# Optimization experiments

Hardware: AMD Instinct MI355X
Metric: run time of the kernel (lower is better)

## Reference

```python
import jax, jax.numpy as jnp
import numpy as np

LEAK = 0.95
NUM_STEPS = 10
THR = 1.0  # all layers get threshold = 1.0 in __init__

@jax.custom_vjp
def spike(x):
    # Surrogate_BP_Function.forward: heaviside(x > 0)
    return (x > 0).astype(x.dtype)

def _spike_fwd(x):
    return spike(x), x

def _spike_bwd(x, g):
    # backward: grad * 0.3 * relu(1 - |x|)
    return (g * 0.3 * jnp.maximum(1.0 - jnp.abs(x), 0.0),)

spike.defvjp(_spike_fwd, _spike_bwd)

def conv3x3(x, w):
    # stride 1, padding 1, no bias, NCHW / OIHW
    return jax.lax.conv_general_dilated(
        x, w, window_strides=(1, 1), padding=[(1, 1), (1, 1)],
        dimension_numbers=('NCHW', 'OIHW', 'NCHW'))

def avgpool2(x):
    b, c, h, w = x.shape
    return x.reshape(b, c, h // 2, 2, w // 2, 2).mean(axis=(3, 5))

def setup_inputs() -> dict:
    key = jax.random.key(0)
    ks = jax.random.split(key, 11)
    def w(k, shape, scale):
        return jax.random.normal(k, shape, dtype=jnp.float32) * scale
    inp = jax.random.normal(ks[0], (128, 3, 32, 32), dtype=jnp.float32)
    return {
        'inp': inp,
        'w1': w(ks[1], (64, 3, 3, 3), 0.35),
        'w2': w(ks[2], (64, 64, 3, 3), 0.1),
        'w3': w(ks[3], (128, 64, 3, 3), 0.1),
        'w4': w(ks[4], (128, 128, 3, 3), 0.08),
        'w5': w(ks[5], (256, 128, 3, 3), 0.08),
        'w6': w(ks[6], (256, 256, 3, 3), 0.06),
        'w7': w(ks[7], (256, 256, 3, 3), 0.06),
        'fc1_w': w(ks[8], (1024, 4096), 0.03),   # Linear(4*4*256, 1024)
        'fc2_w': w(ks[9], (10, 1024), 0.05),     # Linear(1024, 10)
    }

def reference(inp, w1, w2, w3, w4, w5, w6, w7, fc1_w, fc2_w):
    batch = inp.shape[0]
    conv_ws = [w2, w3, w4, w5, w6, w7]          # layers i = 1..6
    pool_after = [True, False, True, False, False, True]  # pool1 after i=1, pool2 after i=3, pool3 after i=6
    static = conv3x3(inp, w1)                   # static_input = conv1(inp)

    def step(carry, _):
        mem0, mem_fc1, mem_fc2 = carry
        # LIF update for conv1 (leaky accumulation of static input)
        mem0 = (1.0 - LEAK) * mem0 + LEAK * static
        thr = mem0 / THR - 1.0
        out_prev = spike(thr)
        mem0 = mem0 - jnp.where(thr > 0, THR, 0.0)  # soft reset
        # conv layers 2..7: membrane is OVERWRITTEN by the conv output each step
        for j, w in enumerate(conv_ws):
            m = conv3x3(out_prev, w)
            thr = m / THR - 1.0
            out_prev = spike(thr)
            if pool_after[j]:
                out_prev = avgpool2(out_prev)
        flat = out_prev.reshape(batch, -1)      # [B, 256*4*4]
        mem_fc1 = (1.0 - LEAK) * mem_fc1 + LEAK * (flat @ fc1_w.T)
        thr = mem_fc1 / THR - 1.0
        out = spike(thr)
        mem_fc1 = mem_fc1 - jnp.where(thr > 0, THR, 0.0)
        mem_fc2 = mem_fc2 + out @ fc2_w.T
        return (mem0, mem_fc1, mem_fc2), None

    init = (jnp.zeros_like(static),
            jnp.zeros((batch, 1024), dtype=inp.dtype),
            jnp.zeros((batch, fc2_w.shape[0]), dtype=inp.dtype))
    (mem0, mem_fc1, mem_fc2), _ = jax.lax.scan(step, init, None, length=NUM_STEPS)
    return mem_fc2 / NUM_STEPS
```

## Files before the change

### kernel.cpp

```cpp
#include <hip/hip_runtime.h>


typedef __attribute__((ext_vector_type(4))) int int32x4;

__device__ __forceinline__ float bf2f(ushort h) {
    union { unsigned u; float f; } v; v.u = ((unsigned)h) << 16;
    return v.f;
}
constexpr int ilog2(int x) { int r = 0; while (x > 1) { x >>= 1; ++r; } return r; }

__device__ __forceinline__ void gl_lds16(const void* g, void* l) {
    __builtin_amdgcn_global_load_lds(
        (const __attribute__((address_space(1))) unsigned int*)g,
        (__attribute__((address_space(3))) unsigned int*)l, 16, 0, 0);
}

#define SC21 4.76837158203125e-07
#define SC23 1.1920928955078125e-07

template <int IC, int OC>
__global__ void prep_convw_i8_k(const float* __restrict__ w, char* __restrict__ dst) {
    int idx = blockIdx.x * 256 + threadIdx.x;
    if (idx >= OC * IC * 9) return;
    int oc = idx / (IC * 9);
    int rem = idx % (IC * 9);
    int ic = rem / 9, q = rem % 9;
    int wq_ = (int)rintf(w[idx] * 2097152.0f);
    int a2 = ((wq_ + 128) & 255) - 128;
    int t2 = (wq_ - a2) >> 8;
    int a1 = ((t2 + 128) & 255) - 128;
    int a0 = (t2 - a1) >> 8;
    int sg = ic >> 6, kin = ic & 63, c = kin >> 4, bb = kin & 15;
    int oct = oc >> 6, ocl = oc & 63;
    constexpr int OCT = OC / 64;
    size_t base = ((size_t)(sg * 9 + q) * OCT + oct) * 12288;
    char digs[3] = {(char)a0, (char)a1, (char)a2};
#pragma unroll
    for (int s = 0; s < 3; ++s)
        dst[base + (size_t)(c * 192 + s * 64 + ocl) * 16 + bb] = digs[s];
}

__global__ void prep_fc1w_i8_k(const float* __restrict__ w, char* __restrict__ dst) {
    int idx = blockIdx.x * 256 + threadIdx.x;
    if (idx >= 1024 * 4096) return;
    int j = idx >> 12, k = idx & 4095;
    int c = k >> 4, hw = k & 15;
    int kp = hw * 256 + c;
    int wq_ = (int)rintf(w[idx] * 2097152.0f);
    int a2 = ((wq_ + 128) & 255) - 128;
    int t2 = (wq_ - a2) >> 8;
    int a1 = ((t2 + 128) & 255) - 128;
    int a0 = (t2 - a1) >> 8;
    int slab = kp >> 6, kin = kp & 63, cch = kin >> 4, bb = kin & 15;
    int oct = j >> 6, ocl = j & 63;
    size_t base = ((size_t)(slab * 16 + oct)) * 12288;
    char digs[3] = {(char)a0, (char)a1, (char)a2};
#pragma unroll
    for (int s = 0; s < 3; ++s)
        dst[base + (size_t)(cch * 192 + s * 64 + ocl) * 16 + bb] = digs[s];
}

template <int H, int C>
__global__ void halo0_k(char* __restrict__ buf) {
    constexpr int P = 4 * H + 4;
    constexpr int CPI = P * (C / 16);
    int idx = blockIdx.x * 256 + threadIdx.x;
    if (idx >= 1280 * CPI) return;
    int n = idx / CPI, r = idx % CPI;
    int p = r / (C / 16), c16 = r % (C / 16);
    int row, col;
    if (p < 2 * (H + 2)) { row = (p < H + 2) ? 0 : H + 1; col = p % (H + 2); }
    else { int qq = p - 2 * (H + 2); col = (qq < H) ? 0 : H + 1; row = 1 + (qq % H); }
    *(uint4*)&buf[(((size_t)n * (H + 2) + row) * (H + 2) + col) * C + c16 * 16] =
        (uint4){0u, 0u, 0u, 0u};
}

__global__ __launch_bounds__(256) void conv1lif_k(const float* __restrict__ inp,
                                                  const float* __restrict__ w1,
                                                  char* __restrict__ act1) {
    __shared__ float ws[27 * 64];
    for (int e = threadIdx.x; e < 1728; e += 256) {
        int oc = e / 27, j = e % 27;
        ws[j * 64 + oc] = w1[e];
    }
    __syncthreads();
    int t = blockIdx.x * 256 + threadIdx.x;
    int q = t & 3;
    int m = t >> 2;
    int n = m >> 10, h = (m >> 5) & 31, w = m & 31;
    float xv[27];
#pragma unroll
    for (int ic = 0; ic < 3; ++ic)
#pragma unroll
        for (int kh = 0; kh < 3; ++kh)
#pragma unroll
            for (int kw = 0; kw < 3; ++kw) {
                int r = h + kh - 1, c = w + kw - 1;
                xv[ic * 9 + kh * 3 + kw] =
                    (r >= 0 && r < 32 && c >= 0 && c < 32)
                        ? inp[(n * 3 + ic) * 1024 + r * 32 + c] : 0.0f;
            }
    float s[16], mem[16];
#pragma unroll
    for (int o = 0; o < 16; ++o) { s[o] = 0.f; mem[o] = 0.f; }
#pragma unroll
    for (int j = 0; j < 27; ++j) {
        float x = xv[j];
        const float* wr = &ws[j * 64 + q * 16];
#pragma unroll
        for (int o = 0; o < 16; ++o) s[o] += wr[o] * x;
    }
    const size_t dbase = (((size_t)h + 1) * 34 + (w + 1)) * 64 + q * 16;
    for (int st = 0; st < 10; ++st) {
        unsigned r[4];
#pragma unroll
        for (int g = 0; g < 4; ++g) {
            unsigned acc = 0;
#pragma unroll
            for (int e = 0; e < 4; ++e) {
                int o = g * 4 + e;
                mem[o] = 0.05f * mem[o] + 0.95f * s[o];
                unsigned b = (mem[o] > 1.f) ? 1u : 0u;
                mem[o] -= (float)b;
                acc |= b << (8 * e);
            }
            r[g] = acc;
        }
        size_t d = ((size_t)(st * 128 + n) * 34 * 34) * 64 + dbase;
        *(uint4*)&act1[d] = (uint4){r[0], r[1], r[2], r[3]};
    }
}

template <int H, int W, int IC, int OC, int NI, int MR, int EPI>
__global__ __launch_bounds__(256, 3) void convi8_k(const char* __restrict__ act,
                                                   const char* __restrict__ wq,
                                                   char* __restrict__ outs,
                                                   float scale) {
    constexpr int PW = W + 2, PHR = MR + 2;
    constexpr int MBLK = NI * MR * W;
    constexpr int NPIX = NI * PHR * PW;
    constexpr int ACH = NPIX * 4;
    constexpr int HR = (ACH + 255) / 256;
    constexpr int SLABS = IC / 64;
    constexpr int OCT = OC / 64;
    constexpr int U = SLABS * 9;
    constexpr int LHW = ilog2(H * W), LW2 = ilog2(W), LMW = ilog2(MR * W);
    static_assert(MBLK == 128, "tile mapping");

    __shared__ __align__(16) char sA[NPIX * 64];
    __shared__ __align__(16) char sB[2][12288];

    const int tid = threadIdx.x, lane = tid & 63;
    const int wid = tid >> 6;
    const int wm = wid >> 1, wn = wid & 1;
    const int b = blockIdx.x, oct = blockIdx.y;
    const int oc0 = oct * 64;
    const int m0 = b * MBLK;
    constexpr int TPI = (NI == 1) ? (H / MR) : 1;
    const int n0 = (NI == 1) ? (b / TPI) : (b * NI);
    const int h0 = (NI == 1) ? (b % TPI) * MR : 0;

    int asrc[HR]; bool apred[HR];
#pragma unroll
    for (int r = 0; r < HR; ++r) {
        int i = r * 256 + tid;
        apred[r] = (i < ACH);
        int ii = apred[r] ? i : 0;
        int c = ii / NPIX, pix = ii % NPIX;
        int pc = pix % PW, t2 = pix / PW;
        int hp = t2 % PHR, img = t2 / PHR;
        asrc[r] = (((n0 + img) * (H + 2) + h0 + hp) * PW + pc) * IC + c * 16;
    }
    const int lan15 = lane & 15;
    int apix[4];
#pragma unroll
    for (int am = 0; am < 4; ++am) {
        int p = wm * 64 + am * 16 + lan15;
        int img = p >> LMW;
        int pi = p & ((MR * W) - 1);
        int h = pi >> LW2;
        apix[am] = (img * PHR + h) * PW + (pi & (W - 1));
    }
    const int cA = lane >> 4;

    int32x4 acc[3][4][2];
#pragma unroll
    for (int s = 0; s < 3; ++s)
#pragma unroll
        for (int a = 0; a < 4; ++a)
#pragma unroll
            for (int bn = 0; bn < 2; ++bn) acc[s][a][bn] = (int32x4){0, 0, 0, 0};

    const size_t wqoct = (size_t)oct * 12288;
    constexpr size_t USTRIDE = (size_t)OCT * 12288;

    auto stage_B = [&](int unit, int bufc) {
        const char* wsrc = wq + (size_t)unit * USTRIDE + wqoct + tid * 16;
        char* d = sB[bufc] + tid * 16;
        gl_lds16(wsrc, d);
        gl_lds16(wsrc + 4096, d + 4096);
        gl_lds16(wsrc + 8192, d + 8192);
    };
    auto stage_A = [&](int sl_) {
#pragma unroll
        for (int r = 0; r < HR; ++r)
            if (apred[r]) gl_lds16(act + asrc[r] + sl_ * 64, sA + (r * 256 + tid) * 16);
    };

    stage_A(0);
    stage_B(0, 0);
    __syncthreads();

    int buf = 0;
    for (int u = 0; u < U; ++u) {
        const int q = u - (u / 9) * 9;
        if (u + 1 < U) stage_B(u + 1, buf ^ 1);
        const int qr = q / 3, qc = q - qr * 3;
        int32x4 af[4];
#pragma unroll
        for (int am = 0; am < 4; ++am)
            af[am] = *(const int32x4*)&sA[(cA * NPIX + apix[am] + qr * PW + qc) * 16];
        __builtin_amdgcn_s_setprio(1);
#pragma unroll
        for (int s = 0; s < 3; ++s)
#pragma unroll
            for (int bn = 0; bn < 2; ++bn) {
                int R = s * 64 + wn * 32 + bn * 16 + lan15;
                int32x4 bf = *(const int32x4*)&sB[buf][(cA * 192 + R) * 16];
#pragma unroll
                for (int am = 0; am < 4; ++am)
                    acc[s][am][bn] = __builtin_amdgcn_mfma_i32_16x16x64_i8(
                        af[am], bf, acc[s][am][bn], 0, 0, 0);
            }
        __builtin_amdgcn_s_setprio(0);
        __syncthreads();
        buf ^= 1;
        if (q == 8 && u + 1 < U) {
            stage_A(u / 9 + 1);
            __syncthreads();
        }
    }

    const double dscale = (double)scale;
#pragma unroll
    for (int am = 0; am < 4; ++am)
#pragma unroll
        for (int bn = 0; bn < 2; ++bn)
#pragma unroll
            for (int rr = 0; rr < 4; ++rr) {
                int rl = wm * 64 + am * 16 + (lane >> 4) * 4 + rr;
                int col = oc0 + wn * 32 + bn * 16 + lan15;
                int m = m0 + rl;
                long long S = ((long long)acc[0][am][bn][rr] << 16)
                            + ((long long)acc[1][am][bn][rr] << 8)
                            + (long long)acc[2][am][bn][rr];
                float v = (float)((double)S * dscale);
                char sp = (v > 1.0f) ? (char)1 : (char)0;
                if (EPI == 1) {
                    int n = m >> LHW, h = (m >> LW2) & (H - 1), w = m & (W - 1);
                    outs[((size_t)(n * (H + 2) + h + 1) * PW + (w + 1)) * OC + col] = sp;
                } else {
                    outs[(size_t)m * OC + col] = sp;
                }
            }
}

template <int C, int HI>
__global__ void pool_i8_k(const char* __restrict__ in, char* __restrict__ out) {
    constexpr int HO = HI / 2, C16 = C / 16;
    constexpr int TOT = 1280 * HO * HO * C16;
    int idx = blockIdx.x * 256 + threadIdx.x;
    if (idx >= TOT) return;
    int c16 = idx % C16;
    int t = idx / C16;
    int w = t % HO; t /= HO;
    int h = t % HO;
    int n = t / HO;
    const char* p = in + ((size_t)(n * HI + 2 * h) * HI + 2 * w) * C + c16 * 16;
    uint4 a0 = *(const uint4*)p;
    uint4 a1 = *(const uint4*)(p + C);
    uint4 a2 = *(const uint4*)(p + (size_t)HI * C);
    uint4 a3 = *(const uint4*)(p + (size_t)HI * C + C);
    uint4 r;
    r.x = a0.x + a1.x + a2.x + a3.x;
    r.y = a0.y + a1.y + a2.y + a3.y;
    r.z = a0.z + a1.z + a2.z + a3.z;
    r.w = a0.w + a1.w + a2.w + a3.w;
    *(uint4*)&out[((size_t)(n * (HO + 2) + h + 1) * (HO + 2) + (w + 1)) * C + c16 * 16] = r;
}

__global__ void pool3q_k(const char* __restrict__ in, char* __restrict__ out) {
    int idx = blockIdx.x * 256 + threadIdx.x;
    if (idx >= 327680) return;
    int c16 = idx & 15;
    int t = idx >> 4;
    int wo = t & 3, ho = (t >> 2) & 3, n = t >> 4;
    const char* p = in + ((size_t)(n * 8 + 2 * ho) * 8 + 2 * wo) * 256 + c16 * 16;
    uint4 a0 = *(const uint4*)p;
    uint4 a1 = *(const uint4*)(p + 256);
    uint4 a2 = *(const uint4*)(p + 2048);
    uint4 a3 = *(const uint4*)(p + 2048 + 256);
    uint4 r;
    r.x = a0.x + a1.x + a2.x + a3.x;
    r.y = a0.y + a1.y + a2.y + a3.y;
    r.z = a0.z + a1.z + a2.z + a3.z;
    r.w = a0.w + a1.w + a2.w + a3.w;
    *(uint4*)&out[((size_t)(n * 16 + ho * 4 + wo) * 16 + c16) * 16] = r;
}

__global__ __launch_bounds__(256) void fc1i8_k(const char* __restrict__ A,
                                               const char* __restrict__ wq,
                                               float* __restrict__ part) {
    __shared__ __align__(16) char sA[2][8192];
    __shared__ __align__(16) char sB[2][12288];
    const int tid = threadIdx.x, lane = tid & 63;
    const int wid = tid >> 6, wm = wid >> 1, wn = wid & 1;
    const int m0 = blockIdx.x * 128, oct = blockIdx.y, kt = blockIdx.z;

    int32x4 acc[3][4][2];
#pragma unroll
    for (int s = 0; s < 3; ++s)
#pragma unroll
        for (int a = 0; a < 4; ++a)
#pragma unroll
            for (int bn = 0; bn < 2; ++bn) acc[s][a][bn] = (int32x4){0, 0, 0, 0};

    auto stageA = [&](int sg, int bf_) {
#pragma unroll
        for (int r = 0; r < 2; ++r) {
            int i = r * 256 + tid;
            int c = i >> 7, pix = i & 127;
            gl_lds16(A + (size_t)(m0 + pix) * 4096 + sg * 64 + c * 16,
                     sA[bf_] + (size_t)i * 16);
        }
    };
    auto stageB = [&](int sg, int bf_) {
        const char* src = wq + ((size_t)(sg * 16 + oct)) * 12288 + tid * 16;
#pragma unroll
        for (int r = 0; r < 3; ++r)
            gl_lds16(src + r * 4096, sB[bf_] + (r * 256 + tid) * 16);
    };

    int buf = 0;
    stageA(kt * 32, 0);
    stageB(kt * 32, 0);
    __syncthreads();
    const int cA = lane >> 4;
    for (int sl = 0; sl < 32; ++sl) {
        int sg = kt * 32 + sl;
        if (sl < 31) { stageA(sg + 1, buf ^ 1); stageB(sg + 1, buf ^ 1); }
        int32x4 af[4];
#pragma unroll
        for (int am = 0; am < 4; ++am)
            af[am] = *(const int32x4*)&sA[buf][(cA * 128 + wm * 64 + am * 16 + (lane & 15)) * 16];
#pragma unroll
        for (int s = 0; s < 3; ++s)
#pragma unroll
            for (int bn = 0; bn < 2; ++bn) {
                int R = s * 64 + wn * 32 + bn * 16 + (lane & 15);
                int32x4 bf = *(const int32x4*)&sB[buf][(cA * 192 + R) * 16];
#pragma unroll
                for (int am = 0; am < 4; ++am)
                    acc[s][am][bn] = __builtin_amdgcn_mfma_i32_16x16x64_i8(
                        af[am], bf, acc[s][am][bn], 0, 0, 0);
            }
        if (sl < 31) { __syncthreads(); buf ^= 1; }
    }
#pragma unroll
    for (int am = 0; am < 4; ++am)
#pragma unroll
        for (int bn = 0; bn < 2; ++bn)
#pragma unroll
            for (int rr = 0; rr < 4; ++rr) {
                int row = m0 + wm * 64 + am * 16 + (lane >> 4) * 4 + rr;
                int col = oct * 64 + wn * 32 + bn * 16 + (lane & 15);
                long long S = ((long long)acc[0][am][bn][rr] << 16)
                            + ((long long)acc[1][am][bn][rr] << 8)
                            + (long long)acc[2][am][bn][rr];
                part[((size_t)kt * 1280 + row) * 1024 + col] = (float)((double)S * SC23);
            }
}

__global__ void fc1lif_k(const float* __restrict__ part, ushort* __restrict__ sbuf) {
    int idx = blockIdx.x * 256 + threadIdx.x;
    int n = idx >> 10, j = idx & 1023;
    float m = 0.f;
    for (int t = 0; t < 10; ++t) {
        size_t row = (size_t)(t * 128 + n) * 1024 + j;
        float y = part[row] + part[1310720 + row];
        m = 0.05f * m + 0.95f * y;
        float sp = (m > 1.f) ? 1.f : 0.f;
        m -= sp;
        sbuf[row] = sp > 0.f ? (ushort)0x3F80 : (ushort)0;
    }
}

__global__ __launch_bounds__(256) void fc2o_k(const ushort* __restrict__ S,
                                              const float* __restrict__ W2,
                                              float* __restrict__ out) {
    __shared__ float wsh[10 * 1024];
    __shared__ float red[10][256];
    int n = blockIdx.x, tid = threadIdx.x;
    for (int e = tid; e < 10240; e += 256) wsh[e] = W2[e];
    __syncthreads();
    float accv = 0.f;
    for (int t = 0; t < 10; ++t) {
        const ushort* sp = S + ((size_t)(t * 128 + n)) * 1024 + tid * 4;
        float s0 = bf2f(sp[0]), s1 = bf2f(sp[1]), s2 = bf2f(sp[2]), s3 = bf2f(sp[3]);
#pragma unroll
        for (int o = 0; o < 10; ++o) {
            const float* w = &wsh[o * 1024 + tid * 4];
            red[o][tid] = s0 * w[0] + s1 * w[1] + s2 * w[2] + s3 * w[3];
        }
        __syncthreads();
        for (int off = 128; off >= 1; off >>= 1) {
            if (tid < off) {
#pragma unroll
                for (int o = 0; o < 10; ++o) red[o][tid] += red[o][tid + off];
            }
            __syncthreads();
        }
        if (tid < 10) accv += red[tid][0];
        __syncthreads();
    }
    if (tid < 10) out[n * 10 + tid] = accv * 0.1f;
}

extern "C" void kernel_launch(void* const* d_in, const int* in_sizes, int n_in,
                              void* d_out, int out_size, void* d_ws, size_t ws_size,
                              hipStream_t stream) {
    const float* inp  = (const float*)d_in[0];
    const float* w1   = (const float*)d_in[1];
    const float* w2   = (const float*)d_in[2];
    const float* w3   = (const float*)d_in[3];
    const float* w4   = (const float*)d_in[4];
    const float* w5   = (const float*)d_in[5];
    const float* w6   = (const float*)d_in[6];
    const float* w7   = (const float*)d_in[7];
    const float* fc1w = (const float*)d_in[8];
    const float* fc2w = (const float*)d_in[9];
    float* out = (float*)d_out;

    char* base = (char*)d_ws;
    char* arenaA = base;
    char* arenaB = base + 94679040;
    size_t o = 94679040 + 83886080;
    auto alloc = [&](size_t bytes) { void* p = base + o; o += (bytes + 255) & ~(size_t)255; return p; };
    char*   wq2  = (char*)alloc(110592);
    char*   wq3  = (char*)alloc(221184);
    char*   wq4  = (char*)alloc(442368);
    char*   wq5  = (char*)alloc(884736);
    char*   wq6  = (char*)alloc(1769472);
    char*   wq7  = (char*)alloc(1769472);
    char*   wqf1 = (char*)alloc(12582912);
    ushort* sbuf = (ushort*)alloc(2621440);
    (void)ws_size;

    char*  act1  = arenaA;
    char*  c2out = arenaB;
    char*  act2  = arenaA;
    char*  c3out = arenaB;
    char*  c4out = arenaA;
    char*  act3  = arenaA + 41943040;
    char*  c5out = arenaB;
    char*  c6out = arenaB + 33554432;
    char*  c7out = arenaA;
    char*  afc1  = arenaA + 20971520;
    float* part  = (float*)(arenaA + 26214400);

    prep_convw_i8_k<64, 64>  <<<(36864 + 255) / 256, 256, 0, stream>>>(w2, wq2);
    prep_convw_i8_k<64, 128> <<<(73728 + 255) / 256, 256, 0, stream>>>(w3, wq3);
    prep_convw_i8_k<128, 128><<<(147456 + 255) / 256, 256, 0, stream>>>(w4, wq4);
    prep_convw_i8_k<128, 256><<<(294912 + 255) / 256, 256, 0, stream>>>(w5, wq5);
    prep_convw_i8_k<256, 256><<<(589824 + 255) / 256, 256, 0, stream>>>(w6, wq6);
    prep_convw_i8_k<256, 256><<<(589824 + 255) / 256, 256, 0, stream>>>(w7, wq7);
    prep_fc1w_i8_k<<<(4194304 + 255) / 256, 256, 0, stream>>>(fc1w, wqf1);

    halo0_k<32, 64><<<(1280 * 132 * 4 + 255) / 256, 256, 0, stream>>>(act1);
    conv1lif_k<<<2048, 256, 0, stream>>>(inp, w1, act1);

    convi8_k<32, 32, 64, 64, 1, 4, 0>
        <<<dim3(10240, 1), 256, 0, stream>>>(act1, wq2, c2out, (float)SC21);
    halo0_k<16, 64><<<(1280 * 68 * 4 + 255) / 256, 256, 0, stream>>>(act2);
    pool_i8_k<64, 32><<<(1280 * 256 * 4 + 255) / 256, 256, 0, stream>>>(c2out, act2);

    halo0_k<16, 128><<<(1280 * 68 * 8 + 255) / 256, 256, 0, stream>>>(c3out);
    convi8_k<16, 16, 64, 128, 1, 8, 1>
        <<<dim3(2560, 2), 256, 0, stream>>>(act2, wq3, c3out, (float)SC23);
    convi8_k<16, 16, 128, 128, 1, 8, 0>
        <<<dim3(2560, 2), 256, 0, stream>>>(c3out, wq4, c4out, (float)SC21);
    halo0_k<8, 128><<<(1280 * 36 * 8 + 255) / 256, 256, 0, stream>>>(act3);
    pool_i8_k<128, 16><<<(1280 * 64 * 8 + 255) / 256, 256, 0, stream>>>(c4out, act3);

    halo0_k<8, 256><<<(1280 * 36 * 16 + 255) / 256, 256, 0, stream>>>(c5out);
    convi8_k<8, 8, 128, 256, 2, 8, 1>
        <<<dim3(640, 4), 256, 0, stream>>>(act3, wq5, c5out, (float)SC23);
    halo0_k<8, 256><<<(1280 * 36 * 16 + 255) / 256, 256, 0, stream>>>(c6out);
    convi8_k<8, 8, 256, 256, 2, 8, 1>
        <<<dim3(640, 4), 256, 0, stream>>>(c5out, wq6, c6out, (float)SC21);
    convi8_k<8, 8, 256, 256, 2, 8, 0>
        <<<dim3(640, 4), 256, 0, stream>>>(c6out, wq7, c7out, (float)SC21);

    pool3q_k<<<(327680 + 255) / 256, 256, 0, stream>>>(c7out, afc1);

    fc1i8_k<<<dim3(10, 16, 2), 256, 0, stream>>>(afc1, wqf1, part);
    fc1lif_k<<<512, 256, 0, stream>>>(part, sbuf);
    fc2o_k<<<128, 256, 0, stream>>>(sbuf, fc2w, out);
}
```

Before: 796.0 us.

## Triple-buffer conv weight tiles with manual vmcnt waits and single barrier

Adds a third LDS buffer for int8 weight tiles so loads run two taps ahead, and replaces the per-tap __syncthreads with an explicit s_waitcnt vmcnt(3) plus one s_barrier at the top of each tap. The tap loop is split into slab/row/column loops with precomputed LDS base offsets, which removes per-iteration index arithmetic. The intent is to hide global-to-LDS weight load latency and cut barrier overhead. It costs 12KB more LDS per block, which may reduce occupancy at launch_bounds 3, and it depends on the hand-written waitcnt counts being correct with the A-slab restaging.

Result: slower. 817.6 us (+2.7%).

```diff
diff --git a/kernel.cpp b/kernel.cpp
--- a/kernel.cpp
+++ b/kernel.cpp
@@ -148,7 +148,7 @@
     static_assert(MBLK == 128, "tile mapping");
 
     __shared__ __align__(16) char sA[NPIX * 64];
-    __shared__ __align__(16) char sB[2][12288];
+    __shared__ __align__(16) char sB[3][12288];
 
     const int tid = threadIdx.x, lane = tid & 63;
     const int wid = tid >> 6;
@@ -172,16 +172,17 @@
         asrc[r] = (((n0 + img) * (H + 2) + h0 + hp) * PW + pc) * IC + c * 16;
     }
     const int lan15 = lane & 15;
-    int apix[4];
+    const int cA = lane >> 4;
+    int afbase[4];
 #pragma unroll
     for (int am = 0; am < 4; ++am) {
         int p = wm * 64 + am * 16 + lan15;
         int img = p >> LMW;
         int pi = p & ((MR * W) - 1);
         int h = pi >> LW2;
-        apix[am] = (img * PHR + h) * PW + (pi & (W - 1));
-    }
-    const int cA = lane >> 4;
+        afbase[am] = (cA * NPIX + (img * PHR + h) * PW + (pi & (W - 1))) * 16;
+    }
+    const int bfb = (cA * 192 + wn * 32 + lan15) * 16;
 
     int32x4 acc[3][4][2];
 #pragma unroll
@@ -191,15 +192,15 @@
 #pragma unroll
             for (int bn = 0; bn < 2; ++bn) acc[s][a][bn] = (int32x4){0, 0, 0, 0};
 
-    const size_t wqoct = (size_t)oct * 12288;
     constexpr size_t USTRIDE = (size_t)OCT * 12288;
-
-    auto stage_B = [&](int unit, int bufc) {
-        const char* wsrc = wq + (size_t)unit * USTRIDE + wqoct + tid * 16;
+    const char* wqbase = wq + (size_t)oct * 12288;
+
+    auto stage_Bp = [&](const char* wsrc, int bufc) {
+        const char* s = wsrc + tid * 16;
         char* d = sB[bufc] + tid * 16;
-        gl_lds16(wsrc, d);
-        gl_lds16(wsrc + 4096, d + 4096);
-        gl_lds16(wsrc + 8192, d + 8192);
+        gl_lds16(s, d);
+        gl_lds16(s + 4096, d + 4096);
+        gl_lds16(s + 8192, d + 8192);
     };
     auto stage_A = [&](int sl_) {
 #pragma unroll
@@ -208,36 +209,56 @@
     };
 
     stage_A(0);
-    stage_B(0, 0);
-    __syncthreads();
-
-    int buf = 0;
-    for (int u = 0; u < U; ++u) {
-        const int q = u - (u / 9) * 9;
-        if (u + 1 < U) stage_B(u + 1, buf ^ 1);
-        const int qr = q / 3, qc = q - qr * 3;
-        int32x4 af[4];
-#pragma unroll
-        for (int am = 0; am < 4; ++am)
-            af[am] = *(const int32x4*)&sA[(cA * NPIX + apix[am] + qr * PW + qc) * 16];
-        __builtin_amdgcn_s_setprio(1);
-#pragma unroll
-        for (int s = 0; s < 3; ++s)
-#pragma unroll
-            for (int bn = 0; bn < 2; ++bn) {
-                int R = s * 64 + wn * 32 + bn * 16 + lan15;
-                int32x4 bf = *(const int32x4*)&sB[buf][(cA * 192 + R) * 16];
+    stage_Bp(wqbase, 0);
+    if (U > 1) stage_Bp(wqbase + USTRIDE, 1);
+    const char* wnext = wqbase + 2 * USTRIDE;
+
+    int buf = 0, u = 0;
+    for (int sl = 0; sl < SLABS; ++sl) {
+        for (int qr = 0; qr < 3; ++qr) {
+            const int rowoff = qr * (PW * 16);
+            for (int qc = 0; qc < 3; ++qc) {
+                if (qr == 0 && qc == 0)
+                    asm volatile("s_waitcnt vmcnt(0)" ::: "memory");
+                else
+                    asm volatile("s_waitcnt vmcnt(3)" ::: "memory");
+                __builtin_amdgcn_s_barrier();
+                asm volatile("" ::: "memory");
+                if (u + 2 < U) {
+                    int b2 = buf + 2;
+                    if (b2 >= 3) b2 -= 3;
+                    stage_Bp(wnext, b2);
+                    wnext += USTRIDE;
+                }
+                const int tapoff = rowoff + qc * 16;
+                int32x4 af[4];
 #pragma unroll
                 for (int am = 0; am < 4; ++am)
-                    acc[s][am][bn] = __builtin_amdgcn_mfma_i32_16x16x64_i8(
-                        af[am], bf, acc[s][am][bn], 0, 0, 0);
-            }
-        __builtin_amdgcn_s_setprio(0);
-        __syncthreads();
-        buf ^= 1;
-        if (q == 8 && u + 1 < U) {
-            stage_A(u / 9 + 1);
-            __syncthreads();
+                    af[am] = *(const int32x4*)&sA[afbase[am] + tapoff];
+                const char* bb = sB[buf] + bfb;
+                __builtin_amdgcn_s_setprio(1);
+#pragma unroll
+                for (int s = 0; s < 3; ++s)
+#pragma unroll
+                    for (int bn = 0; bn < 2; ++bn) {
+                        int32x4 bf = *(const int32x4*)(bb + s * 1024 + bn * 256);
+#pragma unroll
+                        for (int am = 0; am < 4; ++am)
+                            acc[s][am][bn] = __builtin_amdgcn_mfma_i32_16x16x64_i8(
+                                af[am], bf, acc[s][am][bn], 0, 0, 0);
+                    }
+                __builtin_amdgcn_s_setprio(0);
+                if (qr == 2 && qc == 2 && sl + 1 < SLABS) {
+                    asm volatile("s_waitcnt lgkmcnt(0)" ::: "memory");
+                    __builtin_amdgcn_s_barrier();
+                    asm volatile("" ::: "memory");
+                    stage_A(sl + 1);
+                }
+                int bn_ = buf + 1;
+                if (bn_ >= 3) bn_ -= 3;
+                buf = bn_;
+                ++u;
+            }
         }
     }
 
```
